# Kernel tuning notes

Hardware: AMD Instinct MI355X
Metric: run time of the kernel (lower is better)

Reference implementation:

```python
import jax, jax.numpy as jnp
import numpy as np


def _ln(x, g, b, eps=1e-5):
    m = x.mean(-1, keepdims=True)
    v = x.var(-1, keepdims=True)
    return (x - m) / jnp.sqrt(v + eps) * g + b


def setup_inputs() -> dict:
    key = jax.random.key(0)
    ks = jax.random.split(key, 10)
    N, H, E, OUT, L = 4096, 256, 131072, 64, 6
    s = 1.0 / np.sqrt(H)
    return {
        "x": jax.random.normal(ks[0], (N, H), jnp.float32),
        "edge_index": jax.random.randint(ks[1], (2, E), 0, N, jnp.int32),
        "sage_wl": jax.random.normal(ks[2], (L, H, H), jnp.float32) * s,   # lin_l (neighbors, has bias)
        "sage_wr": jax.random.normal(ks[3], (L, H, H), jnp.float32) * s,   # lin_r (root, no bias)
        "sage_bl": jnp.zeros((L, H), jnp.float32),
        "ln_g": jnp.ones((L - 1, H), jnp.float32),
        "ln_b": jnp.zeros((L - 1, H), jnp.float32),
        "conv_w": jax.random.normal(ks[4], (3, H, H, 3), jnp.float32) * (1.0 / np.sqrt(3 * H)),  # [layer,O,I,K]
        "conv_b": jnp.zeros((3, H), jnp.float32),
        "cnorm_g": jnp.ones((3, H), jnp.float32),
        "cnorm_b": jnp.zeros((3, H), jnp.float32),
        "in_proj_w": jax.random.normal(ks[5], (6 * H, 2 * H), jnp.float32) * (1.0 / np.sqrt(2 * H)),
        "in_proj_b": jnp.zeros((6 * H,), jnp.float32),
        "out_proj_w": jax.random.normal(ks[6], (2 * H, 2 * H), jnp.float32) * (1.0 / np.sqrt(2 * H)),
        "out_proj_b": jnp.zeros((2 * H,), jnp.float32),
        "anorm_g": jnp.ones((2 * H,), jnp.float32),
        "anorm_b": jnp.zeros((2 * H,), jnp.float32),
        "fuse_w": jax.random.normal(ks[7], (OUT, 2 * H), jnp.float32) * (1.0 / np.sqrt(2 * H)),
        "fuse_b": jnp.zeros((OUT,), jnp.float32),
    }


def reference(x, edge_index, sage_wl, sage_wr, sage_bl, ln_g, ln_b,
              conv_w, conv_b, cnorm_g, cnorm_b,
              in_proj_w, in_proj_b, out_proj_w, out_proj_b,
              anorm_g, anorm_b, fuse_w, fuse_b):
    # Dropout layers act as identity (eval mode).
    N, H = x.shape
    L = sage_wl.shape[0]
    src, dst = edge_index[0], edge_index[1]
    deg = jax.ops.segment_sum(jnp.ones(src.shape[0], x.dtype), dst, num_segments=N)
    deg = jnp.maximum(deg, 1.0)[:, None]
    h = x
    for i in range(L):
        res = h
        # SAGEConv: mean-aggregate neighbor features (gather/scatter), then two linears
        agg = jax.ops.segment_sum(h[src], dst, num_segments=N) / deg
        h = agg @ sage_wl[i].T + sage_bl[i] + h @ sage_wr[i].T
        if i < L - 1:
            h = _ln(h, ln_g[i], ln_b[i])
        h = jax.nn.relu(h) + res  # residual (shapes always match: in==hidden)
    gnn_out = h                                   # [N, H]

    # CNN branch over the node axis: [1, H, N]
    c = gnn_out.T[None]
    for j in range(3):
        c = jax.lax.conv_general_dilated(c, conv_w[j], (1,), ((1, 1),),
                                         dimension_numbers=("NCH", "OIH", "NCH"))
        c = jax.nn.relu(c + conv_b[j][None, :, None])
        c = _ln(c.transpose(0, 2, 1), cnorm_g[j], cnorm_b[j]).transpose(0, 2, 1)
    cnn_out = c[0].T                              # [N, H]

    fused = jnp.concatenate([gnn_out, cnn_out], axis=1)  # [N, 2H]
    E2 = fused.shape[1]
    heads = 4
    hd = E2 // heads
    qkv = fused @ in_proj_w.T + in_proj_b
    q, k, v = jnp.split(qkv, 3, axis=1)
    split_heads = lambda t: t.reshape(N, heads, hd).transpose(1, 0, 2)  # [h, N, hd]
    q, k, v = split_heads(q), split_heads(k), split_heads(v)
    scores = jnp.einsum("hnd,hmd->hnm", q, k) / np.sqrt(hd).astype(np.float32)
    a = jax.nn.softmax(scores, axis=-1)
    o = jnp.einsum("hnm,hmd->hnd", a, v).transpose(1, 0, 2).reshape(N, E2)
    o = o @ out_proj_w.T + out_proj_b
    o = _ln(o, anorm_g, anorm_b)
    return o @ fuse_w.T + fuse_b                  # [N, out_channels]
```

## Files before the change

kernel.cpp:

```cpp
#include <hip/hip_runtime.h>

#define NN 4096
#define HH 256
#define EE 131072

__device__ __constant__ float LN_EPS = 1e-5f;
#define ATT_SCALE 0.08838834764831845f
#define ATT_SHIFT 30.0f

typedef __attribute__((ext_vector_type(8))) short bf16x8_t;
typedef __attribute__((ext_vector_type(4))) float f32x4_t;

__device__ inline ushort f2b(float f) {
  uint u = __float_as_uint(f);
  uint r = (u + 0x7FFF + ((u >> 16) & 1)) >> 16;
  return (ushort)r;
}

__global__ void hist_kernel(const int* __restrict__ ei, int* __restrict__ cnt) {
  int e = blockIdx.x * blockDim.x + threadIdx.x;
  if (e < EE) atomicAdd(&cnt[ei[EE + e]], 1);
}

__global__ __launch_bounds__(1024) void scan_kernel(int* __restrict__ cnt_cursor,
                                                    int* __restrict__ rowptr,
                                                    float* __restrict__ invdeg) {
  __shared__ int part[1024];
  int t = threadIdx.x;
  int base = t * 4;
  int cs[4];
  int s = 0;
  for (int u = 0; u < 4; ++u) { cs[u] = cnt_cursor[base + u]; s += cs[u]; }
  part[t] = s;
  __syncthreads();
  for (int off = 1; off < 1024; off <<= 1) {
    int add = (t >= off) ? part[t - off] : 0;
    int v = part[t];
    __syncthreads();
    part[t] = v + add;
    __syncthreads();
  }
  int excl = (t > 0) ? part[t - 1] : 0;
  for (int u = 0; u < 4; ++u) {
    rowptr[base + u] = excl;
    cnt_cursor[base + u] = excl;
    invdeg[base + u] = 1.0f / (float)max(cs[u], 1);
    excl += cs[u];
  }
  if (t == 1023) rowptr[NN] = excl;
}

__global__ void fill_kernel(const int* __restrict__ ei, int* __restrict__ cursor,
                            int* __restrict__ col) {
  int e = blockIdx.x * blockDim.x + threadIdx.x;
  if (e < EE) {
    int d = ei[EE + e];
    int p = atomicAdd(&cursor[d], 1);
    col[p] = ei[e];
  }
}

__global__ __launch_bounds__(256) void castw(const float* __restrict__ in,
                                             ushort* __restrict__ out) {
  int i4 = (blockIdx.x * 256 + threadIdx.x) * 4;
  float4 v = *(const float4*)(in + i4);
  ushort4 w;
  w.x = f2b(v.x); w.y = f2b(v.y); w.z = f2b(v.z); w.w = f2b(v.w);
  *(ushort4*)(out + i4) = w;
}

__global__ __launch_bounds__(256) void castconv(const float* __restrict__ w,
                                                ushort* __restrict__ o) {
  int idx = blockIdx.x * 256 + threadIdx.x;
  int j = idx / 196608;
  int rem = idx - j * 196608;
  int oc = rem / 768;
  int kk = rem - oc * 768;
  int ks = kk >> 8, ii = kk & 255;
  o[idx] = f2b(w[j * 196608 + oc * 768 + ii * 3 + ks]);
}

__global__ __launch_bounds__(64) void agg_kernel(const float* __restrict__ h,
                                                 const int* __restrict__ rowptr,
                                                 const int* __restrict__ col,
                                                 const float* __restrict__ invdeg,
                                                 ushort* __restrict__ aggb) {
  int n = blockIdx.x;
  int t = threadIdx.x;
  int s = rowptr[n], e = rowptr[n + 1];
  float4 acc = make_float4(0.f, 0.f, 0.f, 0.f);
  for (int j = s; j < e; ++j) {
    int c = col[j];
    const float4 v = *(const float4*)(h + (size_t)c * HH + t * 4);
    acc.x += v.x; acc.y += v.y; acc.z += v.z; acc.w += v.w;
  }
  float id = invdeg[n];
  ushort4 w;
  w.x = f2b(acc.x * id); w.y = f2b(acc.y * id);
  w.z = f2b(acc.z * id); w.w = f2b(acc.w * id);
  *(ushort4*)(aggb + (size_t)n * HH + t * 4) = w;
}

__global__ __launch_bounds__(256) void gemm_mfma(
    const ushort* __restrict__ A0, const ushort* __restrict__ A1,
    const ushort* __restrict__ B0, const ushort* __restrict__ B1,
    const float* __restrict__ bias, float* __restrict__ Cf, ushort* __restrict__ Cb,
    int M, int Nn, int K, int KHA, int KHB, int relu) {
  __shared__ ushort Alds[64][40];
  __shared__ ushort Blds[128][40];
  int t = threadIdx.x;
  int w = t >> 6, l = t & 63, quad = l >> 4, lr = l & 15;
  int wm = w & 1, wn = w >> 1;
  int m0 = blockIdx.x * 64, n0 = blockIdx.y * 128;
  int sr = t >> 2, sc8 = (t & 3) * 8;
  f32x4_t acc[2][4];
#pragma unroll
  for (int s = 0; s < 2; ++s)
#pragma unroll
    for (int q = 0; q < 4; ++q) acc[s][q] = (f32x4_t){0.f, 0.f, 0.f, 0.f};

  for (int k0 = 0; k0 < K; k0 += 32) {
    int kk = k0 + sc8;
    const ushort* ap = (kk < KHA) ? (A0 + (size_t)(m0 + sr) * KHA + kk)
                                  : (A1 + (size_t)(m0 + sr) * (K - KHA) + (kk - KHA));
    uint4 av = *(const uint4*)ap;
    const ushort* bp0 = (kk < KHB) ? (B0 + (size_t)(n0 + sr) * KHB + kk)
                                   : (B1 + (size_t)(n0 + sr) * (K - KHB) + (kk - KHB));
    uint4 bv0 = *(const uint4*)bp0;
    const ushort* bp1 = (kk < KHB) ? (B0 + (size_t)(n0 + 64 + sr) * KHB + kk)
                                   : (B1 + (size_t)(n0 + 64 + sr) * (K - KHB) + (kk - KHB));
    uint4 bv1 = *(const uint4*)bp1;
    __syncthreads();
    *(uint4*)&Alds[sr][sc8] = av;
    *(uint4*)&Blds[sr][sc8] = bv0;
    *(uint4*)&Blds[64 + sr][sc8] = bv1;
    __syncthreads();
    bf16x8_t af[2], bf[4];
#pragma unroll
    for (int s = 0; s < 2; ++s)
      af[s] = *(const bf16x8_t*)&Alds[wm * 32 + s * 16 + lr][quad * 8];
#pragma unroll
    for (int q = 0; q < 4; ++q)
      bf[q] = *(const bf16x8_t*)&Blds[wn * 64 + q * 16 + lr][quad * 8];
#pragma unroll
    for (int s = 0; s < 2; ++s)
#pragma unroll
      for (int q = 0; q < 4; ++q)
        acc[s][q] = __builtin_amdgcn_mfma_f32_16x16x32_bf16(af[s], bf[q], acc[s][q], 0, 0, 0);
  }
#pragma unroll
  for (int s = 0; s < 2; ++s) {
#pragma unroll
    for (int q = 0; q < 4; ++q) {
      int n = n0 + wn * 64 + q * 16 + lr;
      float bb = bias[n];
#pragma unroll
      for (int r = 0; r < 4; ++r) {
        int m = m0 + wm * 32 + s * 16 + quad * 4 + r;
        float v = acc[s][q][r] + bb;
        if (relu) v = fmaxf(v, 0.f);
        if (Cf) Cf[(size_t)m * Nn + n] = v;
        if (Cb) Cb[(size_t)m * Nn + n] = f2b(v);
      }
    }
  }
}

__global__ __launch_bounds__(256) void gemm_conv_mfma(
    const ushort* __restrict__ Ab, const ushort* __restrict__ B,
    const float* __restrict__ bias, float* __restrict__ Cf) {
  __shared__ ushort Alds[64][40];
  __shared__ ushort Blds[128][40];
  int t = threadIdx.x;
  int w = t >> 6, l = t & 63, quad = l >> 4, lr = l & 15;
  int wm = w & 1, wn = w >> 1;
  int m0 = blockIdx.x * 64, n0 = blockIdx.y * 128;
  int sr = t >> 2, sc8 = (t & 3) * 8;
  f32x4_t acc[2][4];
#pragma unroll
  for (int s = 0; s < 2; ++s)
#pragma unroll
    for (int q = 0; q < 4; ++q) acc[s][q] = (f32x4_t){0.f, 0.f, 0.f, 0.f};

  for (int k0 = 0; k0 < 768; k0 += 32) {
    int kk = k0 + sc8;
    int ks = kk >> 8, ii = kk & 255;
    int nr = m0 + sr + ks - 1;
    uint4 av = make_uint4(0u, 0u, 0u, 0u);
    if (nr >= 0 && nr < NN) av = *(const uint4*)(Ab + (size_t)nr * HH + ii);
    uint4 bv0 = *(const uint4*)(B + (size_t)(n0 + sr) * 768 + kk);
    uint4 bv1 = *(const uint4*)(B + (size_t)(n0 + 64 + sr) * 768 + kk);
    __syncthreads();
    *(uint4*)&Alds[sr][sc8] = av;
    *(uint4*)&Blds[sr][sc8] = bv0;
    *(uint4*)&Blds[64 + sr][sc8] = bv1;
    __syncthreads();
    bf16x8_t af[2], bf[4];
#pragma unroll
    for (int s = 0; s < 2; ++s)
      af[s] = *(const bf16x8_t*)&Alds[wm * 32 + s * 16 + lr][quad * 8];
#pragma unroll
    for (int q = 0; q < 4; ++q)
      bf[q] = *(const bf16x8_t*)&Blds[wn * 64 + q * 16 + lr][quad * 8];
#pragma unroll
    for (int s = 0; s < 2; ++s)
#pragma unroll
      for (int q = 0; q < 4; ++q)
        acc[s][q] = __builtin_amdgcn_mfma_f32_16x16x32_bf16(af[s], bf[q], acc[s][q], 0, 0, 0);
  }
#pragma unroll
  for (int s = 0; s < 2; ++s) {
#pragma unroll
    for (int q = 0; q < 4; ++q) {
      int n = n0 + wn * 64 + q * 16 + lr;
      float bb = bias[n];
#pragma unroll
      for (int r = 0; r < 4; ++r) {
        int m = m0 + wm * 32 + s * 16 + quad * 4 + r;
        Cf[(size_t)m * HH + n] = fmaxf(acc[s][q][r] + bb, 0.f);
      }
    }
  }
}

__global__ __launch_bounds__(256) void gemm_std(
    const float* __restrict__ A0, const float* __restrict__ B0,
    const float* __restrict__ bias, float* __restrict__ C,
    int M, int Nn, int K) {
  __shared__ float As[16][68];
  __shared__ float Bs[16][68];
  int t = threadIdx.x;
  int m0 = blockIdx.x * 64, n0 = blockIdx.y * 64;
  int ty = t >> 4, tx = t & 15;
  int lr = t >> 2, lc4 = (t & 3) * 4;
  float acc[4][4] = {};
  for (int k0 = 0; k0 < K; k0 += 16) {
    int kk = k0 + lc4;
    float4 va = *(const float4*)(A0 + (size_t)(m0 + lr) * K + kk);
    As[lc4 + 0][lr] = va.x; As[lc4 + 1][lr] = va.y;
    As[lc4 + 2][lr] = va.z; As[lc4 + 3][lr] = va.w;
    float4 vb = *(const float4*)(B0 + (size_t)(n0 + lr) * K + kk);
    Bs[lc4 + 0][lr] = vb.x; Bs[lc4 + 1][lr] = vb.y;
    Bs[lc4 + 2][lr] = vb.z; Bs[lc4 + 3][lr] = vb.w;
    __syncthreads();
#pragma unroll
    for (int k = 0; k < 16; ++k) {
      float4 a4 = *(const float4*)&As[k][4 * ty];
      float4 b4 = *(const float4*)&Bs[k][4 * tx];
      float av[4] = {a4.x, a4.y, a4.z, a4.w};
      float bv[4] = {b4.x, b4.y, b4.z, b4.w};
#pragma unroll
      for (int i = 0; i < 4; ++i)
#pragma unroll
        for (int j = 0; j < 4; ++j) acc[i][j] += av[i] * bv[j];
    }
    __syncthreads();
  }
#pragma unroll
  for (int i = 0; i < 4; ++i) {
    int m = m0 + 4 * ty + i;
    float o[4];
#pragma unroll
    for (int j = 0; j < 4; ++j) o[j] = acc[i][j] + bias[n0 + 4 * tx + j];
    float4 o4 = make_float4(o[0], o[1], o[2], o[3]);
    *(float4*)(C + (size_t)m * Nn + n0 + 4 * tx) = o4;
  }
}

__global__ __launch_bounds__(256) void ln_fuse(
    const float* __restrict__ x, const float* __restrict__ g, const float* __restrict__ b,
    const float* __restrict__ res, float* __restrict__ outf, ushort* __restrict__ outb,
    int D, int do_ln, int relu_res) {
  int row = blockIdx.x, t = threadIdx.x;
  int nv = D >> 8;
  float vals[2];
  float s = 0.f, sq = 0.f;
  for (int u = 0; u < nv; ++u) {
    float v = x[(size_t)row * D + t + (u << 8)];
    vals[u] = v; s += v; sq += v * v;
  }
  __shared__ float red[8];
  float m = 0.f, inv = 1.f;
  if (do_ln) {
    for (int off = 32; off >= 1; off >>= 1) {
      s += __shfl_xor(s, off);
      sq += __shfl_xor(sq, off);
    }
    int wid = t >> 6;
    if ((t & 63) == 0) { red[wid] = s; red[4 + wid] = sq; }
    __syncthreads();
    if (t == 0) {
      float S = red[0] + red[1] + red[2] + red[3];
      float Q = red[4] + red[5] + red[6] + red[7];
      float mm = S / D;
      float vv = Q / D - mm * mm;
      red[0] = mm;
      red[1] = rsqrtf(vv + LN_EPS);
    }
    __syncthreads();
    m = red[0]; inv = red[1];
  }
  for (int u = 0; u < nv; ++u) {
    int c = t + (u << 8);
    float y = vals[u];
    if (do_ln) y = (y - m) * inv * g[c] + b[c];
    if (relu_res) y = fmaxf(y, 0.f) + res[(size_t)row * D + c];
    if (outf) outf[(size_t)row * D + c] = y;
    if (outb) outb[(size_t)row * D + c] = f2b(y);
  }
}

__global__ __launch_bounds__(256) void vtrans(const ushort* __restrict__ qkvb,
                                              ushort* __restrict__ Vt) {
  __shared__ ushort tile[32][34];
  int t = threadIdx.x;
  int n0 = blockIdx.x * 32, d0 = blockIdx.y * 32;
  int tx = t & 31, ty = t >> 5;
#pragma unroll
  for (int u = 0; u < 4; ++u) {
    int r = ty + 8 * u;
    tile[r][tx] = qkvb[(size_t)(n0 + r) * 1536 + 1024 + d0 + tx];
  }
  __syncthreads();
#pragma unroll
  for (int u = 0; u < 4; ++u) {
    int dy = ty + 8 * u;
    Vt[(size_t)(d0 + dy) * NN + n0 + tx] = tile[tx][dy];
  }
}

__global__ __launch_bounds__(128) void attn_mfma(const ushort* __restrict__ qkvb,
                                                 const ushort* __restrict__ Vt,
                                                 ushort* __restrict__ Ob) {
  __shared__ ushort Klds[64][136];
  __shared__ ushort Vlds[128][72];
  __shared__ ushort Plds[2][16][72];

  int t = threadIdx.x;
  int w = t >> 6, l = t & 63;
  int quad = l >> 4, lr = l & 15;
  int head = blockIdx.y;
  int q0 = blockIdx.x * 32;

  bf16x8_t qf[4];
#pragma unroll
  for (int ks = 0; ks < 4; ++ks)
    qf[ks] = *(const bf16x8_t*)(qkvb + (size_t)(q0 + w * 16 + lr) * 1536 + head * 128 +
                                ks * 32 + quad * 8);

  f32x4_t of[8];
#pragma unroll
  for (int dt = 0; dt < 8; ++dt) of[dt] = (f32x4_t){0.f, 0.f, 0.f, 0.f};
  float den[4] = {0.f, 0.f, 0.f, 0.f};

  for (int kt = 0; kt < NN / 64; ++kt) {
    int k0 = kt * 64;
    __syncthreads();
#pragma unroll
    for (int p = 0; p < 8; ++p) {
      int c0 = t + p * 128;
      int row = c0 >> 4, c8 = (c0 & 15) * 8;
      *(uint4*)&Klds[row][c8] =
          *(const uint4*)(qkvb + (size_t)(k0 + row) * 1536 + 512 + head * 128 + c8);
    }
#pragma unroll
    for (int p = 0; p < 8; ++p) {
      int c0 = t + p * 128;
      int row = c0 >> 3, kv8 = (c0 & 7) * 8;
      *(uint4*)&Vlds[row][kv8] =
          *(const uint4*)(Vt + (size_t)(head * 128 + row) * NN + k0 + kv8);
    }
    __syncthreads();

    f32x4_t sf[4];
#pragma unroll
    for (int ct = 0; ct < 4; ++ct) sf[ct] = (f32x4_t){0.f, 0.f, 0.f, 0.f};
#pragma unroll
    for (int ks = 0; ks < 4; ++ks) {
#pragma unroll
      for (int ct = 0; ct < 4; ++ct) {
        bf16x8_t kf = *(const bf16x8_t*)&Klds[ct * 16 + lr][ks * 32 + quad * 8];
        sf[ct] = __builtin_amdgcn_mfma_f32_16x16x32_bf16(qf[ks], kf, sf[ct], 0, 0, 0);
      }
    }

    float rs[4] = {0.f, 0.f, 0.f, 0.f};
#pragma unroll
    for (int ct = 0; ct < 4; ++ct) {
#pragma unroll
      for (int r = 0; r < 4; ++r) {
        float e = __expf(sf[ct][r] * ATT_SCALE - ATT_SHIFT);
        Plds[w][quad * 4 + r][ct * 16 + lr] = f2b(e);
        rs[r] += e;
      }
    }
#pragma unroll
    for (int mask = 1; mask < 16; mask <<= 1) {
#pragma unroll
      for (int r = 0; r < 4; ++r) rs[r] += __shfl_xor(rs[r], mask);
    }
#pragma unroll
    for (int r = 0; r < 4; ++r) den[r] += rs[r];

#pragma unroll
    for (int ks2 = 0; ks2 < 2; ++ks2) {
      bf16x8_t pf = *(const bf16x8_t*)&Plds[w][lr][ks2 * 32 + quad * 8];
#pragma unroll
      for (int dt = 0; dt < 8; ++dt) {
        bf16x8_t vf = *(const bf16x8_t*)&Vlds[dt * 16 + lr][ks2 * 32 + quad * 8];
        of[dt] = __builtin_amdgcn_mfma_f32_16x16x32_bf16(pf, vf, of[dt], 0, 0, 0);
      }
    }
  }

  float inv[4];
#pragma unroll
  for (int r = 0; r < 4; ++r) inv[r] = 1.0f / den[r];
#pragma unroll
  for (int dt = 0; dt < 8; ++dt) {
#pragma unroll
    for (int r = 0; r < 4; ++r) {
      int row = q0 + w * 16 + quad * 4 + r;
      Ob[(size_t)row * 512 + head * 128 + dt * 16 + lr] = f2b(of[dt][r] * inv[r]);
    }
  }
}

extern "C" void kernel_launch(void* const* d_in, const int* in_sizes, int n_in,
                              void* d_out, int out_size, void* d_ws, size_t ws_size,
                              hipStream_t stream) {
  const float* x          = (const float*)d_in[0];
  const int*   ei         = (const int*)d_in[1];
  const float* sage_wl    = (const float*)d_in[2];
  const float* sage_wr    = (const float*)d_in[3];
  const float* sage_bl    = (const float*)d_in[4];
  const float* ln_g       = (const float*)d_in[5];
  const float* ln_b       = (const float*)d_in[6];
  const float* conv_w     = (const float*)d_in[7];
  const float* conv_b     = (const float*)d_in[8];
  const float* cnorm_g    = (const float*)d_in[9];
  const float* cnorm_b    = (const float*)d_in[10];
  const float* in_proj_w  = (const float*)d_in[11];
  const float* in_proj_b  = (const float*)d_in[12];
  const float* out_proj_w = (const float*)d_in[13];
  const float* out_proj_b = (const float*)d_in[14];
  const float* anorm_g    = (const float*)d_in[15];
  const float* anorm_b    = (const float*)d_in[16];
  const float* fuse_w     = (const float*)d_in[17];
  const float* fuse_b     = (const float*)d_in[18];
  float* out = (float*)d_out;

  char* ws = (char*)d_ws;
  const size_t MB = 1 << 20;
  int*    rowptr = (int*)(ws + 0);
  int*    cnt    = (int*)(ws + 65536);
  int*    col    = (int*)(ws + 131072);
  float*  invdeg = (float*)(ws + 786432);
  float*  h    = (float*)(ws + 1 * MB);
  ushort* hb   = (ushort*)(ws + 5 * MB);
  ushort* aggb = (ushort*)(ws + 7 * MB);
  float*  tmp  = (float*)(ws + 9 * MB);
  ushort* c0b  = (ushort*)(ws + 13 * MB);
  ushort* c1b  = (ushort*)(ws + 15 * MB);
  ushort* qkvb = (ushort*)(ws + 17 * MB);
  float*  op   = (float*)(ws + 17 * MB);
  ushort* Vt   = (ushort*)(ws + 29 * MB);
  ushort* aob  = (ushort*)(ws + 33 * MB);
  ushort* wlb  = (ushort*)(ws + 37 * MB);
  ushort* wrb  = (ushort*)(ws + 37 * MB + 786432);
  ushort* cvb  = (ushort*)(ws + 37 * MB + 1572864);
  ushort* ipb  = (ushort*)(ws + 37 * MB + 2752512);
  ushort* opb  = (ushort*)(ws + 37 * MB + 4325376);

  castw<<<(6 * 256 * 256) / 1024, 256, 0, stream>>>(sage_wl, wlb);
  castw<<<(6 * 256 * 256) / 1024, 256, 0, stream>>>(sage_wr, wrb);
  castconv<<<(3 * 256 * 768) / 256, 256, 0, stream>>>(conv_w, cvb);
  castw<<<(1536 * 512) / 1024, 256, 0, stream>>>(in_proj_w, ipb);
  castw<<<(512 * 512) / 1024, 256, 0, stream>>>(out_proj_w, opb);

  hipMemsetAsync(cnt, 0, NN * sizeof(int), stream);
  hist_kernel<<<EE / 256, 256, 0, stream>>>(ei, cnt);
  scan_kernel<<<1, 1024, 0, stream>>>(cnt, rowptr, invdeg);
  fill_kernel<<<EE / 256, 256, 0, stream>>>(ei, cnt, col);
  hipMemcpyAsync(h, x, (size_t)NN * HH * sizeof(float), hipMemcpyDeviceToDevice, stream);
  castw<<<(NN * HH) / 1024, 256, 0, stream>>>(x, hb);

  for (int i = 0; i < 6; ++i) {
    agg_kernel<<<NN, 64, 0, stream>>>(h, rowptr, col, invdeg, aggb);
    gemm_mfma<<<dim3(64, 2), 256, 0, stream>>>(
        aggb, hb, wlb + (size_t)i * HH * HH, wrb + (size_t)i * HH * HH,
        sage_bl + i * HH, tmp, nullptr, NN, HH, 512, 256, 256, 0);
    int do_ln = (i < 5) ? 1 : 0;
    const float* gp = do_ln ? (ln_g + i * HH) : ln_g;
    const float* bp = do_ln ? (ln_b + i * HH) : ln_b;
    ln_fuse<<<NN, 256, 0, stream>>>(tmp, gp, bp, h, h, hb, HH, do_ln, 1);
  }

  const ushort* cin = hb;
  ushort* couts[3] = {c0b, c1b, c0b};
  for (int j = 0; j < 3; ++j) {
    gemm_conv_mfma<<<dim3(64, 2), 256, 0, stream>>>(
        cin, cvb + (size_t)j * HH * 768, conv_b + j * HH, tmp);
    ln_fuse<<<NN, 256, 0, stream>>>(tmp, cnorm_g + j * HH, cnorm_b + j * HH,
                                    nullptr, nullptr, couts[j], HH, 1, 0);
    cin = couts[j];
  }

  gemm_mfma<<<dim3(64, 12), 256, 0, stream>>>(
      hb, c0b, ipb, nullptr, in_proj_b, nullptr, qkvb, NN, 1536, 512, 256, 1536 * 0 + 512, 0);
  vtrans<<<dim3(NN / 32, 512 / 32), 256, 0, stream>>>(qkvb, Vt);
  attn_mfma<<<dim3(NN / 32, 4), 128, 0, stream>>>(qkvb, Vt, aob);

  gemm_mfma<<<dim3(64, 4), 256, 0, stream>>>(
      aob, nullptr, opb, nullptr, out_proj_b, op, nullptr, NN, 512, 512, 512, 512, 0);
  ln_fuse<<<NN, 256, 0, stream>>>(op, anorm_g, anorm_b, nullptr, op, nullptr, 512, 1, 0);
  gemm_std<<<dim3(64, 1), 256, 0, stream>>>(op, fuse_w, fuse_b, out, NN, 64, 512);
}
```

Baseline: 606.7 us.

## Split attention over KV halves, shrink GEMM tiles, bf16 aggregation, warp-per-row layernorm

```diff
diff --git a/kernel.cpp b/kernel.cpp
--- a/kernel.cpp
+++ b/kernel.cpp
@@ -16,6 +16,7 @@
   uint r = (u + 0x7FFF + ((u >> 16) & 1)) >> 16;
   return (ushort)r;
 }
+__device__ inline float b2f(ushort u) { return __uint_as_float(((uint)u) << 16); }
 
 __global__ void hist_kernel(const int* __restrict__ ei, int* __restrict__ cnt) {
   int e = blockIdx.x * blockDim.x + threadIdx.x;
@@ -80,7 +81,7 @@
   o[idx] = f2b(w[j * 196608 + oc * 768 + ii * 3 + ks]);
 }
 
-__global__ __launch_bounds__(64) void agg_kernel(const float* __restrict__ h,
+__global__ __launch_bounds__(64) void agg_kernel(const ushort* __restrict__ hb,
                                                  const int* __restrict__ rowptr,
                                                  const int* __restrict__ col,
                                                  const float* __restrict__ invdeg,
@@ -88,24 +89,23 @@
   int n = blockIdx.x;
   int t = threadIdx.x;
   int s = rowptr[n], e = rowptr[n + 1];
-  float4 acc = make_float4(0.f, 0.f, 0.f, 0.f);
+  float a0 = 0.f, a1 = 0.f, a2 = 0.f, a3 = 0.f;
   for (int j = s; j < e; ++j) {
     int c = col[j];
-    const float4 v = *(const float4*)(h + (size_t)c * HH + t * 4);
-    acc.x += v.x; acc.y += v.y; acc.z += v.z; acc.w += v.w;
+    ushort4 u = *(const ushort4*)(hb + (size_t)c * HH + t * 4);
+    a0 += b2f(u.x); a1 += b2f(u.y); a2 += b2f(u.z); a3 += b2f(u.w);
   }
   float id = invdeg[n];
   ushort4 w;
-  w.x = f2b(acc.x * id); w.y = f2b(acc.y * id);
-  w.z = f2b(acc.z * id); w.w = f2b(acc.w * id);
+  w.x = f2b(a0 * id); w.y = f2b(a1 * id); w.z = f2b(a2 * id); w.w = f2b(a3 * id);
   *(ushort4*)(aggb + (size_t)n * HH + t * 4) = w;
 }
 
 __global__ __launch_bounds__(256) void gemm_mfma(
     const ushort* __restrict__ A0, const ushort* __restrict__ A1,
-    const ushort* __restrict__ B0, const ushort* __restrict__ B1,
+    const ushort* __restrict__ B0,
     const float* __restrict__ bias, float* __restrict__ Cf, ushort* __restrict__ Cb,
-    int M, int Nn, int K, int KHA, int KHB, int relu) {
+    int M, int Nn, int K, int KHA) {
   __shared__ ushort Alds[64][40];
   __shared__ ushort Blds[128][40];
   int t = threadIdx.x;
@@ -124,12 +124,8 @@
     const ushort* ap = (kk < KHA) ? (A0 + (size_t)(m0 + sr) * KHA + kk)
                                   : (A1 + (size_t)(m0 + sr) * (K - KHA) + (kk - KHA));
     uint4 av = *(const uint4*)ap;
-    const ushort* bp0 = (kk < KHB) ? (B0 + (size_t)(n0 + sr) * KHB + kk)
-                                   : (B1 + (size_t)(n0 + sr) * (K - KHB) + (kk - KHB));
-    uint4 bv0 = *(const uint4*)bp0;
-    const ushort* bp1 = (kk < KHB) ? (B0 + (size_t)(n0 + 64 + sr) * KHB + kk)
-                                   : (B1 + (size_t)(n0 + 64 + sr) * (K - KHB) + (kk - KHB));
-    uint4 bv1 = *(const uint4*)bp1;
+    uint4 bv0 = *(const uint4*)(B0 + (size_t)(n0 + sr) * K + kk);
+    uint4 bv1 = *(const uint4*)(B0 + (size_t)(n0 + 64 + sr) * K + kk);
     __syncthreads();
     *(uint4*)&Alds[sr][sc8] = av;
     *(uint4*)&Blds[sr][sc8] = bv0;
@@ -158,9 +154,66 @@
       for (int r = 0; r < 4; ++r) {
         int m = m0 + wm * 32 + s * 16 + quad * 4 + r;
         float v = acc[s][q][r] + bb;
-        if (relu) v = fmaxf(v, 0.f);
         if (Cf) Cf[(size_t)m * Nn + n] = v;
         if (Cb) Cb[(size_t)m * Nn + n] = f2b(v);
+      }
+    }
+  }
+}
+
+__global__ __launch_bounds__(256) void gemm_mfma64(
+    const ushort* __restrict__ A0, const ushort* __restrict__ A1,
+    const ushort* __restrict__ B0, const ushort* __restrict__ B1,
+    const float* __restrict__ bias, float* __restrict__ Cf,
+    int M, int Nn, int K, int KHA, int KHB) {
+  __shared__ ushort Alds[64][40];
+  __shared__ ushort Blds[64][40];
+  int t = threadIdx.x;
+  int w = t >> 6, l = t & 63, quad = l >> 4, lr = l & 15;
+  int wm = w & 1, wn = w >> 1;
+  int m0 = blockIdx.x * 64, n0 = blockIdx.y * 64;
+  int sr = t >> 2, sc8 = (t & 3) * 8;
+  f32x4_t acc[2][2];
+#pragma unroll
+  for (int s = 0; s < 2; ++s)
+#pragma unroll
+    for (int q = 0; q < 2; ++q) acc[s][q] = (f32x4_t){0.f, 0.f, 0.f, 0.f};
+
+  for (int k0 = 0; k0 < K; k0 += 32) {
+    int kk = k0 + sc8;
+    const ushort* ap = (kk < KHA) ? (A0 + (size_t)(m0 + sr) * KHA + kk)
+                                  : (A1 + (size_t)(m0 + sr) * (K - KHA) + (kk - KHA));
+    uint4 av = *(const uint4*)ap;
+    const ushort* bp = (kk < KHB) ? (B0 + (size_t)(n0 + sr) * KHB + kk)
+                                  : (B1 + (size_t)(n0 + sr) * (K - KHB) + (kk - KHB));
+    uint4 bv = *(const uint4*)bp;
+    __syncthreads();
+    *(uint4*)&Alds[sr][sc8] = av;
+    *(uint4*)&Blds[sr][sc8] = bv;
+    __syncthreads();
+    bf16x8_t af[2], bf[2];
+#pragma unroll
+    for (int s = 0; s < 2; ++s)
+      af[s] = *(const bf16x8_t*)&Alds[wm * 32 + s * 16 + lr][quad * 8];
+#pragma unroll
+    for (int q = 0; q < 2; ++q)
+      bf[q] = *(const bf16x8_t*)&Blds[wn * 32 + q * 16 + lr][quad * 8];
+#pragma unroll
+    for (int s = 0; s < 2; ++s)
+#pragma unroll
+      for (int q = 0; q < 2; ++q)
+        acc[s][q] = __builtin_amdgcn_mfma_f32_16x16x32_bf16(af[s], bf[q], acc[s][q], 0, 0, 0);
+  }
+#pragma unroll
+  for (int s = 0; s < 2; ++s) {
+#pragma unroll
+    for (int q = 0; q < 2; ++q) {
+      int n = n0 + wn * 32 + q * 16 + lr;
+      float bb = bias[n];
+#pragma unroll
+      for (int r = 0; r < 4; ++r) {
+        int m = m0 + wm * 32 + s * 16 + quad * 4 + r;
+        Cf[(size_t)m * Nn + n] = acc[s][q][r] + bb;
       }
     }
   }
@@ -170,17 +223,17 @@
     const ushort* __restrict__ Ab, const ushort* __restrict__ B,
     const float* __restrict__ bias, float* __restrict__ Cf) {
   __shared__ ushort Alds[64][40];
-  __shared__ ushort Blds[128][40];
+  __shared__ ushort Blds[64][40];
   int t = threadIdx.x;
   int w = t >> 6, l = t & 63, quad = l >> 4, lr = l & 15;
   int wm = w & 1, wn = w >> 1;
-  int m0 = blockIdx.x * 64, n0 = blockIdx.y * 128;
+  int m0 = blockIdx.x * 64, n0 = blockIdx.y * 64;
   int sr = t >> 2, sc8 = (t & 3) * 8;
-  f32x4_t acc[2][4];
+  f32x4_t acc[2][2];
 #pragma unroll
   for (int s = 0; s < 2; ++s)
 #pragma unroll
-    for (int q = 0; q < 4; ++q) acc[s][q] = (f32x4_t){0.f, 0.f, 0.f, 0.f};
+    for (int q = 0; q < 2; ++q) acc[s][q] = (f32x4_t){0.f, 0.f, 0.f, 0.f};
 
   for (int k0 = 0; k0 < 768; k0 += 32) {
     int kk = k0 + sc8;
@@ -188,31 +241,29 @@
     int nr = m0 + sr + ks - 1;
     uint4 av = make_uint4(0u, 0u, 0u, 0u);
     if (nr >= 0 && nr < NN) av = *(const uint4*)(Ab + (size_t)nr * HH + ii);
-    uint4 bv0 = *(const uint4*)(B + (size_t)(n0 + sr) * 768 + kk);
-    uint4 bv1 = *(const uint4*)(B + (size_t)(n0 + 64 + sr) * 768 + kk);
+    uint4 bv = *(const uint4*)(B + (size_t)(n0 + sr) * 768 + kk);
     __syncthreads();
     *(uint4*)&Alds[sr][sc8] = av;
-    *(uint4*)&Blds[sr][sc8] = bv0;
-    *(uint4*)&Blds[64 + sr][sc8] = bv1;
-    __syncthreads();
-    bf16x8_t af[2], bf[4];
+    *(uint4*)&Blds[sr][sc8] = bv;
+    __syncthreads();
+    bf16x8_t af[2], bf[2];
 #pragma unroll
     for (int s = 0; s < 2; ++s)
       af[s] = *(const bf16x8_t*)&Alds[wm * 32 + s * 16 + lr][quad * 8];
 #pragma unroll
-    for (int q = 0; q < 4; ++q)
-      bf[q] = *(const bf16x8_t*)&Blds[wn * 64 + q * 16 + lr][quad * 8];
+    for (int q = 0; q < 2; ++q)
+      bf[q] = *(const bf16x8_t*)&Blds[wn * 32 + q * 16 + lr][quad * 8];
 #pragma unroll
     for (int s = 0; s < 2; ++s)
 #pragma unroll
-      for (int q = 0; q < 4; ++q)
+      for (int q = 0; q < 2; ++q)
         acc[s][q] = __builtin_amdgcn_mfma_f32_16x16x32_bf16(af[s], bf[q], acc[s][q], 0, 0, 0);
   }
 #pragma unroll
   for (int s = 0; s < 2; ++s) {
 #pragma unroll
-    for (int q = 0; q < 4; ++q) {
-      int n = n0 + wn * 64 + q * 16 + lr;
+    for (int q = 0; q < 2; ++q) {
+      int n = n0 + wn * 32 + q * 16 + lr;
       float bb = bias[n];
 #pragma unroll
       for (int r = 0; r < 4; ++r) {
@@ -223,90 +274,54 @@
   }
 }
 
-__global__ __launch_bounds__(256) void gemm_std(
-    const float* __restrict__ A0, const float* __restrict__ B0,
-    const float* __restrict__ bias, float* __restrict__ C,
-    int M, int Nn, int K) {
-  __shared__ float As[16][68];
-  __shared__ float Bs[16][68];
-  int t = threadIdx.x;
-  int m0 = blockIdx.x * 64, n0 = blockIdx.y * 64;
-  int ty = t >> 4, tx = t & 15;
-  int lr = t >> 2, lc4 = (t & 3) * 4;
-  float acc[4][4] = {};
-  for (int k0 = 0; k0 < K; k0 += 16) {
-    int kk = k0 + lc4;
-    float4 va = *(const float4*)(A0 + (size_t)(m0 + lr) * K + kk);
-    As[lc4 + 0][lr] = va.x; As[lc4 + 1][lr] = va.y;
-    As[lc4 + 2][lr] = va.z; As[lc4 + 3][lr] = va.w;
-    float4 vb = *(const float4*)(B0 + (size_t)(n0 + lr) * K + kk);
-    Bs[lc4 + 0][lr] = vb.x; Bs[lc4 + 1][lr] = vb.y;
-    Bs[lc4 + 2][lr] = vb.z; Bs[lc4 + 3][lr] = vb.w;
-    __syncthreads();
-#pragma unroll
-    for (int k = 0; k < 16; ++k) {
-      float4 a4 = *(const float4*)&As[k][4 * ty];
-      float4 b4 = *(const float4*)&Bs[k][4 * tx];
-      float av[4] = {a4.x, a4.y, a4.z, a4.w};
-      float bv[4] = {b4.x, b4.y, b4.z, b4.w};
-#pragma unroll
-      for (int i = 0; i < 4; ++i)
-#pragma unroll
-        for (int j = 0; j < 4; ++j) acc[i][j] += av[i] * bv[j];
-    }
-    __syncthreads();
-  }
-#pragma unroll
-  for (int i = 0; i < 4; ++i) {
-    int m = m0 + 4 * ty + i;
-    float o[4];
-#pragma unroll
-    for (int j = 0; j < 4; ++j) o[j] = acc[i][j] + bias[n0 + 4 * tx + j];
-    float4 o4 = make_float4(o[0], o[1], o[2], o[3]);
-    *(float4*)(C + (size_t)m * Nn + n0 + 4 * tx) = o4;
-  }
-}
-
 __global__ __launch_bounds__(256) void ln_fuse(
     const float* __restrict__ x, const float* __restrict__ g, const float* __restrict__ b,
     const float* __restrict__ res, float* __restrict__ outf, ushort* __restrict__ outb,
     int D, int do_ln, int relu_res) {
-  int row = blockIdx.x, t = threadIdx.x;
+  int w = threadIdx.x >> 6, l = threadIdx.x & 63;
+  int row = blockIdx.x * 4 + w;
+  const float* xr = x + (size_t)row * D;
   int nv = D >> 8;
-  float vals[2];
+  float4 v[2];
   float s = 0.f, sq = 0.f;
   for (int u = 0; u < nv; ++u) {
-    float v = x[(size_t)row * D + t + (u << 8)];
-    vals[u] = v; s += v; sq += v * v;
-  }
-  __shared__ float red[8];
+    v[u] = *(const float4*)(xr + l * 4 + (u << 8));
+    s += v[u].x + v[u].y + v[u].z + v[u].w;
+    sq += v[u].x * v[u].x + v[u].y * v[u].y + v[u].z * v[u].z + v[u].w * v[u].w;
+  }
   float m = 0.f, inv = 1.f;
   if (do_ln) {
-    for (int off = 32; off >= 1; off >>= 1) {
+    for (int off = 1; off < 64; off <<= 1) {
       s += __shfl_xor(s, off);
       sq += __shfl_xor(sq, off);
     }
-    int wid = t >> 6;
-    if ((t & 63) == 0) { red[wid] = s; red[4 + wid] = sq; }
-    __syncthreads();
-    if (t == 0) {
-      float S = red[0] + red[1] + red[2] + red[3];
-      float Q = red[4] + red[5] + red[6] + red[7];
-      float mm = S / D;
-      float vv = Q / D - mm * mm;
-      red[0] = mm;
-      red[1] = rsqrtf(vv + LN_EPS);
-    }
-    __syncthreads();
-    m = red[0]; inv = red[1];
+    m = s / D;
+    inv = rsqrtf(sq / D - m * m + LN_EPS);
   }
   for (int u = 0; u < nv; ++u) {
-    int c = t + (u << 8);
-    float y = vals[u];
-    if (do_ln) y = (y - m) * inv * g[c] + b[c];
-    if (relu_res) y = fmaxf(y, 0.f) + res[(size_t)row * D + c];
-    if (outf) outf[(size_t)row * D + c] = y;
-    if (outb) outb[(size_t)row * D + c] = f2b(y);
+    int c = l * 4 + (u << 8);
+    float4 y = v[u];
+    if (do_ln) {
+      float4 gg = *(const float4*)(g + c);
+      float4 bb = *(const float4*)(b + c);
+      y.x = (y.x - m) * inv * gg.x + bb.x;
+      y.y = (y.y - m) * inv * gg.y + bb.y;
+      y.z = (y.z - m) * inv * gg.z + bb.z;
+      y.w = (y.w - m) * inv * gg.w + bb.w;
+    }
+    if (relu_res) {
+      float4 rr = *(const float4*)(res + (size_t)row * D + c);
+      y.x = fmaxf(y.x, 0.f) + rr.x;
+      y.y = fmaxf(y.y, 0.f) + rr.y;
+      y.z = fmaxf(y.z, 0.f) + rr.z;
+      y.w = fmaxf(y.w, 0.f) + rr.w;
+    }
+    if (outf) *(float4*)(outf + (size_t)row * D + c) = y;
+    if (outb) {
+      ushort4 yb;
+      yb.x = f2b(y.x); yb.y = f2b(y.y); yb.z = f2b(y.z); yb.w = f2b(y.w);
+      *(ushort4*)(outb + (size_t)row * D + c) = yb;
+    }
   }
 }
 
@@ -329,18 +344,20 @@
   }
 }
 
-__global__ __launch_bounds__(128) void attn_mfma(const ushort* __restrict__ qkvb,
+__global__ __launch_bounds__(256) void attn_mfma(const ushort* __restrict__ qkvb,
                                                  const ushort* __restrict__ Vt,
-                                                 ushort* __restrict__ Ob) {
+                                                 float* __restrict__ Onum,
+                                                 float* __restrict__ dpart) {
   __shared__ ushort Klds[64][136];
   __shared__ ushort Vlds[128][72];
-  __shared__ ushort Plds[2][16][72];
+  __shared__ ushort Plds[4][16][72];
 
   int t = threadIdx.x;
   int w = t >> 6, l = t & 63;
   int quad = l >> 4, lr = l & 15;
   int head = blockIdx.y;
-  int q0 = blockIdx.x * 32;
+  int q0 = blockIdx.x * 64;
+  int kvs = blockIdx.z;
 
   bf16x8_t qf[4];
 #pragma unroll
@@ -353,20 +370,20 @@
   for (int dt = 0; dt < 8; ++dt) of[dt] = (f32x4_t){0.f, 0.f, 0.f, 0.f};
   float den[4] = {0.f, 0.f, 0.f, 0.f};
 
-  for (int kt = 0; kt < NN / 64; ++kt) {
-    int k0 = kt * 64;
-    __syncthreads();
-#pragma unroll
-    for (int p = 0; p < 8; ++p) {
-      int c0 = t + p * 128;
-      int row = c0 >> 4, c8 = (c0 & 15) * 8;
+  for (int kt = 0; kt < 32; ++kt) {
+    int k0 = kvs * 2048 + kt * 64;
+    __syncthreads();
+#pragma unroll
+    for (int p = 0; p < 4; ++p) {
+      int idx = t + p * 256;
+      int row = idx >> 4, c8 = (idx & 15) * 8;
       *(uint4*)&Klds[row][c8] =
           *(const uint4*)(qkvb + (size_t)(k0 + row) * 1536 + 512 + head * 128 + c8);
     }
 #pragma unroll
-    for (int p = 0; p < 8; ++p) {
-      int c0 = t + p * 128;
-      int row = c0 >> 3, kv8 = (c0 & 7) * 8;
+    for (int p = 0; p < 4; ++p) {
+      int idx = t + p * 256;
+      int row = idx >> 3, kv8 = (idx & 7) * 8;
       *(uint4*)&Vlds[row][kv8] =
           *(const uint4*)(Vt + (size_t)(head * 128 + row) * NN + k0 + kv8);
     }
@@ -413,17 +430,37 @@
     }
   }
 
-  float inv[4];
-#pragma unroll
-  for (int r = 0; r < 4; ++r) inv[r] = 1.0f / den[r];
+  if (lr == 0) {
+#pragma unroll
+    for (int r = 0; r < 4; ++r)
+      dpart[(size_t)(kvs * 4 + head) * NN + q0 + w * 16 + quad * 4 + r] = den[r];
+  }
 #pragma unroll
   for (int dt = 0; dt < 8; ++dt) {
 #pragma unroll
     for (int r = 0; r < 4; ++r) {
       int row = q0 + w * 16 + quad * 4 + r;
-      Ob[(size_t)row * 512 + head * 128 + dt * 16 + lr] = f2b(of[dt][r] * inv[r]);
-    }
-  }
+      Onum[(size_t)kvs * 2097152 + (size_t)row * 512 + head * 128 + dt * 16 + lr] = of[dt][r];
+    }
+  }
+}
+
+__global__ __launch_bounds__(256) void attn_combine(const float* __restrict__ Onum,
+                                                    const float* __restrict__ dpart,
+                                                    ushort* __restrict__ aob) {
+  int idx = blockIdx.x * 256 + threadIdx.x;
+  int row = idx >> 7;
+  int c4 = (idx & 127) * 4;
+  int head = c4 >> 7;
+  float4 a = *(const float4*)(Onum + (size_t)row * 512 + c4);
+  float4 b = *(const float4*)(Onum + 2097152 + (size_t)row * 512 + c4);
+  float inv = 1.0f / (dpart[(size_t)head * NN + row] + dpart[(size_t)(4 + head) * NN + row]);
+  ushort4 o;
+  o.x = f2b((a.x + b.x) * inv);
+  o.y = f2b((a.y + b.y) * inv);
+  o.z = f2b((a.z + b.z) * inv);
+  o.w = f2b((a.w + b.w) * inv);
+  *(ushort4*)(aob + (size_t)row * 512 + c4) = o;
 }
 
 extern "C" void kernel_launch(void* const* d_in, const int* in_sizes, int n_in,
@@ -456,27 +493,32 @@
   int*    cnt    = (int*)(ws + 65536);
   int*    col    = (int*)(ws + 131072);
   float*  invdeg = (float*)(ws + 786432);
+  float*  dpart  = (float*)(ws + 0);
   float*  h    = (float*)(ws + 1 * MB);
   ushort* hb   = (ushort*)(ws + 5 * MB);
   ushort* aggb = (ushort*)(ws + 7 * MB);
   float*  tmp  = (float*)(ws + 9 * MB);
   ushort* c0b  = (ushort*)(ws + 13 * MB);
   ushort* c1b  = (ushort*)(ws + 15 * MB);
+  float*  Onum = (float*)(ws + 1 * MB);
   ushort* qkvb = (ushort*)(ws + 17 * MB);
   float*  op   = (float*)(ws + 17 * MB);
+  ushort* opbf = (ushort*)(ws + 25 * MB);
   ushort* Vt   = (ushort*)(ws + 29 * MB);
   ushort* aob  = (ushort*)(ws + 33 * MB);
   ushort* wlb  = (ushort*)(ws + 37 * MB);
   ushort* wrb  = (ushort*)(ws + 37 * MB + 786432);
   ushort* cvb  = (ushort*)(ws + 37 * MB + 1572864);
   ushort* ipb  = (ushort*)(ws + 37 * MB + 2752512);
-  ushort* opb  = (ushort*)(ws + 37 * MB + 4325376);
+  ushort* wopb = (ushort*)(ws + 37 * MB + 4325376);
+  ushort* fwb  = (ushort*)(ws + 37 * MB + 4849664);
 
   castw<<<(6 * 256 * 256) / 1024, 256, 0, stream>>>(sage_wl, wlb);
   castw<<<(6 * 256 * 256) / 1024, 256, 0, stream>>>(sage_wr, wrb);
   castconv<<<(3 * 256 * 768) / 256, 256, 0, stream>>>(conv_w, cvb);
   castw<<<(1536 * 512) / 1024, 256, 0, stream>>>(in_proj_w, ipb);
-  castw<<<(512 * 512) / 1024, 256, 0, stream>>>(out_proj_w, opb);
+  castw<<<(512 * 512) / 1024, 256, 0, stream>>>(out_proj_w, wopb);
+  castw<<<(64 * 512) / 1024, 256, 0, stream>>>(fuse_w, fwb);
 
   hipMemsetAsync(cnt, 0, NN * sizeof(int), stream);
   hist_kernel<<<EE / 256, 256, 0, stream>>>(ei, cnt);
@@ -486,33 +528,35 @@
   castw<<<(NN * HH) / 1024, 256, 0, stream>>>(x, hb);
 
   for (int i = 0; i < 6; ++i) {
-    agg_kernel<<<NN, 64, 0, stream>>>(h, rowptr, col, invdeg, aggb);
-    gemm_mfma<<<dim3(64, 2), 256, 0, stream>>>(
+    agg_kernel<<<NN, 64, 0, stream>>>(hb, rowptr, col, invdeg, aggb);
+    gemm_mfma64<<<dim3(64, 4), 256, 0, stream>>>(
         aggb, hb, wlb + (size_t)i * HH * HH, wrb + (size_t)i * HH * HH,
-        sage_bl + i * HH, tmp, nullptr, NN, HH, 512, 256, 256, 0);
+        sage_bl + i * HH, tmp, NN, HH, 512, 256, 256);
     int do_ln = (i < 5) ? 1 : 0;
     const float* gp = do_ln ? (ln_g + i * HH) : ln_g;
     const float* bp = do_ln ? (ln_b + i * HH) : ln_b;
-    ln_fuse<<<NN, 256, 0, stream>>>(tmp, gp, bp, h, h, hb, HH, do_ln, 1);
+    ln_fuse<<<NN / 4, 256, 0, stream>>>(tmp, gp, bp, h, h, hb, HH, do_ln, 1);
   }
 
   const ushort* cin = hb;
   ushort* couts[3] = {c0b, c1b, c0b};
   for (int j = 0; j < 3; ++j) {
-    gemm_conv_mfma<<<dim3(64, 2), 256, 0, stream>>>(
+    gemm_conv_mfma<<<dim3(64, 4), 256, 0, stream>>>(
         cin, cvb + (size_t)j * HH * 768, conv_b + j * HH, tmp);
-    ln_fuse<<<NN, 256, 0, stream>>>(tmp, cnorm_g + j * HH, cnorm_b + j * HH,
-                                    nullptr, nullptr, couts[j], HH, 1, 0);
+    ln_fuse<<<NN / 4, 256, 0, stream>>>(tmp, cnorm_g + j * HH, cnorm_b + j * HH,
+                                        nullptr, nullptr, couts[j], HH, 1, 0);
     cin = couts[j];
   }
 
   gemm_mfma<<<dim3(64, 12), 256, 0, stream>>>(
-      hb, c0b, ipb, nullptr, in_proj_b, nullptr, qkvb, NN, 1536, 512, 256, 1536 * 0 + 512, 0);
+      hb, c0b, ipb, in_proj_b, nullptr, qkvb, NN, 1536, 512, 256);
   vtrans<<<dim3(NN / 32, 512 / 32), 256, 0, stream>>>(qkvb, Vt);
-  attn_mfma<<<dim3(NN / 32, 4), 128, 0, stream>>>(qkvb, Vt, aob);
+  attn_mfma<<<dim3(NN / 64, 4, 2), 256, 0, stream>>>(qkvb, Vt, Onum, dpart);
+  attn_combine<<<(NN * 128) / 256, 256, 0, stream>>>(Onum, dpart, aob);
 
   gemm_mfma<<<dim3(64, 4), 256, 0, stream>>>(
-      aob, nullptr, opb, nullptr, out_proj_b, op, nullptr, NN, 512, 512, 512, 512, 0);
-  ln_fuse<<<NN, 256, 0, stream>>>(op, anorm_g, anorm_b, nullptr, op, nullptr, 512, 1, 0);
-  gemm_std<<<dim3(64, 1), 256, 0, stream>>>(op, fuse_w, fuse_b, out, NN, 64, 512);
-}
+      aob, nullptr, wopb, out_proj_b, op, nullptr, NN, 512, 512, 512);
+  ln_fuse<<<NN / 4, 256, 0, stream>>>(op, anorm_g, anorm_b, nullptr, nullptr, opbf, 512, 1, 0);
+  gemm_mfma64<<<dim3(64, 1), 256, 0, stream>>>(
+      opbf, nullptr, fwb, nullptr, fuse_b, out, NN, 64, 512, 512, 512);
+}
```

Result: slower. 679.2 us (+11.9%).
